# Kernel tuning notes

Hardware: AMD Instinct MI355X
Metric: run time of the kernel (lower is better)

Reference implementation:

```python
import jax, jax.numpy as jnp
import numpy as np

EPS = 1e-8  # torch cosine_similarity clamps norms at 1e-8
TEMPERATURE = 0.05


def _normalize(x):
    n = jnp.linalg.norm(x, axis=-1, keepdims=True)
    return x / jnp.maximum(n, EPS)


def setup_inputs() -> dict:
    key = jax.random.key(0)
    k1, k2, k3 = jax.random.split(key, 3)
    N, D = 8192, 256
    return {
        "text_embeddings": jax.random.normal(k1, (N, D), dtype=jnp.float32),
        "text_pos_embeddings": jax.random.normal(k2, (N, D), dtype=jnp.float32),
        "text_neg_embeddings": jax.random.normal(k3, (N, D), dtype=jnp.float32),
    }


def _pair_loss(a, b):
    # PairInBatchNegCoSentLoss(a, b): cos-sim matrix, scale, diag-subtract, LSE
    sim = _normalize(a) @ _normalize(b).T / TEMPERATURE  # [N, N]
    diff = sim - jnp.diagonal(sim)[:, None]
    return jax.nn.logsumexp(diff, axis=1).mean()


def reference(text_embeddings, text_pos_embeddings, text_neg_embeddings):
    e = _normalize(text_embeddings)
    p = _normalize(text_pos_embeddings)
    n = _normalize(text_neg_embeddings)
    sim_pos = jnp.sum(e * p, axis=-1)          # [N]
    sim_neg = e @ n.T                          # [N, N]
    sim = jnp.concatenate([sim_pos[:, None], sim_neg], axis=1) / TEMPERATURE
    diff = sim - sim[:, 0:1]
    loss = jax.nn.logsumexp(diff, axis=1).mean()
    # add_swap_loss=True: pair loss with (pos, anchor) swapped
    loss = loss + _pair_loss(text_pos_embeddings, text_embeddings)
    return loss
```

## Files before the change

### kernel.cpp

```cpp
#include <hip/hip_runtime.h>
#include <stdint.h>

#define N 8192
#define D 256
#define INV_T 20.0f
#define LOG2E 1.44269504088896340736f
#define BM 128
#define BN 128
#define NXB 64

typedef __attribute__((ext_vector_type(16))) float f32x16;
typedef __attribute__((ext_vector_type(4))) int i32x4;
typedef __attribute__((ext_vector_type(8))) int i32x8;

typedef __attribute__((address_space(3))) uint32_t lds_u32;
typedef __attribute__((address_space(1))) const uint32_t gbl_u32;

static __device__ __forceinline__ float fast_exp2(float x) {
  float r;
  asm("v_exp_f32 %0, %1" : "=v"(r) : "v"(x));
  return r;
}

#define DPP_ADD(v, ctrl)                                                      \
  ((v) + __builtin_bit_cast(float, __builtin_amdgcn_update_dpp(               \
             0, __builtin_bit_cast(int, (v)), (ctrl), 0xf, 0xf, true)))

__global__ __launch_bounds__(256) void normalize_kernel(
    const float* __restrict__ e, const float* __restrict__ p, const float* __restrict__ n,
    uint32_t* __restrict__ eb, uint32_t* __restrict__ pb, uint32_t* __restrict__ nb,
    float* __restrict__ cbuf, float* __restrict__ srow, float* __restrict__ out) {
  const int tid = threadIdx.x;
  const int wave = tid >> 6, lane = tid & 63;
  const int row = blockIdx.x * 4 + wave;

  if (tid < 8) srow[blockIdx.x * 8 + tid] = 0.0f;
  if (blockIdx.x == 0 && tid == 0) out[0] = 0.0f;

  const float4 ev = ((const float4*)(e + (size_t)row * D))[lane];
  const float4 pv = ((const float4*)(p + (size_t)row * D))[lane];
  const float4 nv = ((const float4*)(n + (size_t)row * D))[lane];

  float sse = ev.x*ev.x + ev.y*ev.y + ev.z*ev.z + ev.w*ev.w;
  float ssp = pv.x*pv.x + pv.y*pv.y + pv.z*pv.z + pv.w*pv.w;
  float ssn = nv.x*nv.x + nv.y*nv.y + nv.z*nv.z + nv.w*nv.w;
  float dep = ev.x*pv.x + ev.y*pv.y + ev.z*pv.z + ev.w*pv.w;
#pragma unroll
  for (int m = 1; m < 64; m <<= 1) {
    sse += __shfl_xor(sse, m);
    ssp += __shfl_xor(ssp, m);
    ssn += __shfl_xor(ssn, m);
    dep += __shfl_xor(dep, m);
  }
  const float se = 1.0f / fmaxf(sqrtf(sse), 1e-8f);
  const float sp = 1.0f / fmaxf(sqrtf(ssp), 1e-8f);
  const float sn = 1.0f / fmaxf(sqrtf(ssn), 1e-8f);

  int ue = __builtin_amdgcn_cvt_pk_fp8_f32(ev.x*se, ev.y*se, 0, false);
  ue     = __builtin_amdgcn_cvt_pk_fp8_f32(ev.z*se, ev.w*se, ue, true);
  int up = __builtin_amdgcn_cvt_pk_fp8_f32(pv.x*sp, pv.y*sp, 0, false);
  up     = __builtin_amdgcn_cvt_pk_fp8_f32(pv.z*sp, pv.w*sp, up, true);
  int un = __builtin_amdgcn_cvt_pk_fp8_f32(nv.x*sn, nv.y*sn, 0, false);
  un     = __builtin_amdgcn_cvt_pk_fp8_f32(nv.z*sn, nv.w*sn, un, true);
  eb[row * 64 + lane] = (uint32_t)ue;
  pb[row * 64 + lane] = (uint32_t)up;
  nb[row * 64 + lane] = (uint32_t)un;

  if (lane == 0) cbuf[row] = dep * se * sp * INV_T;
}

__global__ __launch_bounds__(256, 3) void simexp_kernel(
    const uint8_t* __restrict__ eb, const uint8_t* __restrict__ pb,
    const uint8_t* __restrict__ nb, const float* __restrict__ cbuf,
    float* __restrict__ srow) {
  __shared__ uint8_t Bs[BN * D];
  __shared__ float cs[BM];

  const int z = blockIdx.z;
  const uint8_t* __restrict__ A = z ? pb : eb;
  const uint8_t* __restrict__ B = z ? eb : nb;

  const int tid = threadIdx.x;
  const int wave = tid >> 6, lane = tid & 63;
  const int lane31 = lane & 31, half = lane >> 5;
  const int rowTile = blockIdx.x * BM, colblk = blockIdx.y;
  const int colTile = colblk * BN;

#pragma unroll
  for (int i = 0; i < 8; ++i) {
    const int c = i * 256 + tid, r = c >> 4, sl = c & 15;
    const int gg = sl ^ (r & 15);
    __builtin_amdgcn_global_load_lds(
        (gbl_u32*)(B + (size_t)(colTile + r) * D + gg * 16),
        (lds_u32*)&Bs[c * 16], 16, 0, 0);
  }

  const int arow = rowTile + wave * 32 + lane31;
  const uint8_t* __restrict__ Arow = A + (size_t)arow * D + half * 32;
  i32x8 afr[4];
#pragma unroll
  for (int s = 0; s < 4; ++s) {
    const i32x4 lo = *(const i32x4*)(Arow + s * 64);
    const i32x4 hi = *(const i32x4*)(Arow + s * 64 + 16);
    afr[s] = (i32x8){lo[0], lo[1], lo[2], lo[3], hi[0], hi[1], hi[2], hi[3]};
  }

  if (tid < BM) cs[tid] = cbuf[rowTile + tid] * LOG2E;

  int bbase[4];
#pragma unroll
  for (int ni = 0; ni < 4; ++ni) {
    const int cl = ni * 32 + lane31;
    bbase[ni] = (cl << 8) ^ ((cl & 15) << 4) ^ (half << 5);
  }

  f32x16 acc[4];
#pragma unroll
  for (int ni = 0; ni < 4; ++ni)
#pragma unroll
    for (int r = 0; r < 16; ++r) acc[ni][r] = 0.0f;

  __syncthreads();

#pragma unroll
  for (int s = 0; s < 4; ++s) {
#pragma unroll
    for (int ni = 0; ni < 4; ++ni) {
      const int alo = bbase[ni] ^ (s << 6);
      const i32x4 blo = *(const i32x4*)&Bs[alo];
      const i32x4 bhi = *(const i32x4*)&Bs[alo ^ 16];
      const i32x8 b = (i32x8){blo[0], blo[1], blo[2], blo[3],
                              bhi[0], bhi[1], bhi[2], bhi[3]};
      acc[ni] = __builtin_amdgcn_mfma_scale_f32_32x32x64_f8f6f4(
          afr[s], b, acc[ni],
          0 , 0 ,
          0, 0x7F7F7F7F , 0, 0x7F7F7F7F );
    }
  }

  const float K2 = INV_T * LOG2E;
#pragma unroll
  for (int reg = 0; reg < 16; ++reg) {
    const int rlocal = (reg & 3) + 8 * (reg >> 2) + 4 * half;
    const int rowl = wave * 32 + rlocal;
    const float cv = cs[rowl];
    float v = fast_exp2(acc[0][reg] * K2 - cv) + fast_exp2(acc[1][reg] * K2 - cv) +
              fast_exp2(acc[2][reg] * K2 - cv) + fast_exp2(acc[3][reg] * K2 - cv);
    v = DPP_ADD(v, 0xB1);
    v = DPP_ADD(v, 0x4E);
    v = DPP_ADD(v, 0x141);
    v = DPP_ADD(v, 0x140);
    v += __builtin_bit_cast(float, __builtin_amdgcn_ds_swizzle(
             __builtin_bit_cast(int, v), 0x401F));
    if (lane31 == 0)
      atomicAdd(&srow[(size_t)z * N + rowTile + rowl], v);
  }
}

__global__ __launch_bounds__(64) void finalize_kernel(const float* __restrict__ srow,
                                                      float* __restrict__ out) {
  const int r = blockIdx.x * 64 + threadIdx.x;
  const float s = srow[r];
  float val = (r >= N) ? logf(s) : log1pf(s);
#pragma unroll
  for (int m = 1; m < 64; m <<= 1) val += __shfl_xor(val, m);
  if (threadIdx.x == 0) atomicAdd(out, val * (1.0f / (float)N));
}

extern "C" void kernel_launch(void* const* d_in, const int* in_sizes, int n_in,
                              void* d_out, int out_size, void* d_ws, size_t ws_size,
                              hipStream_t stream) {
  const float* e = (const float*)d_in[0];
  const float* p = (const float*)d_in[1];
  const float* n = (const float*)d_in[2];

  char* w = (char*)d_ws;
  uint8_t* eb = (uint8_t*)w;
  uint8_t* pb = eb + (size_t)N * D;
  uint8_t* nb = pb + (size_t)N * D;
  float* cbuf = (float*)(nb + (size_t)N * D);
  float* srow = cbuf + N;

  normalize_kernel<<<N / 4, 256, 0, stream>>>(e, p, n, (uint32_t*)eb, (uint32_t*)pb,
                                              (uint32_t*)nb, cbuf, srow,
                                              (float*)d_out);
  simexp_kernel<<<dim3(N / BM, N / BN, 2), 256, 0, stream>>>(eb, pb, nb, cbuf, srow);
  finalize_kernel<<<256, 64, 0, stream>>>(srow, (float*)d_out);
}
```

Baseline: 126.9 us.

## Replace row-sum atomics with per-column-block partials and restructure MFMA loop

```diff
diff --git a/kernel.cpp b/kernel.cpp
--- a/kernel.cpp
+++ b/kernel.cpp
@@ -29,12 +29,11 @@
 __global__ __launch_bounds__(256) void normalize_kernel(
     const float* __restrict__ e, const float* __restrict__ p, const float* __restrict__ n,
     uint32_t* __restrict__ eb, uint32_t* __restrict__ pb, uint32_t* __restrict__ nb,
-    float* __restrict__ cbuf, float* __restrict__ srow, float* __restrict__ out) {
+    float* __restrict__ cbuf, float* __restrict__ out) {
   const int tid = threadIdx.x;
   const int wave = tid >> 6, lane = tid & 63;
   const int row = blockIdx.x * 4 + wave;
 
-  if (tid < 8) srow[blockIdx.x * 8 + tid] = 0.0f;
   if (blockIdx.x == 0 && tid == 0) out[0] = 0.0f;
 
   const float4 ev = ((const float4*)(e + (size_t)row * D))[lane];
@@ -72,7 +71,7 @@
 __global__ __launch_bounds__(256, 3) void simexp_kernel(
     const uint8_t* __restrict__ eb, const uint8_t* __restrict__ pb,
     const uint8_t* __restrict__ nb, const float* __restrict__ cbuf,
-    float* __restrict__ srow) {
+    float* __restrict__ part) {
   __shared__ uint8_t Bs[BN * D];
   __shared__ float cs[BM];
 
@@ -114,54 +113,65 @@
     bbase[ni] = (cl << 8) ^ ((cl & 15) << 4) ^ (half << 5);
   }
 
-  f32x16 acc[4];
-#pragma unroll
-  for (int ni = 0; ni < 4; ++ni)
-#pragma unroll
-    for (int r = 0; r < 16; ++r) acc[ni][r] = 0.0f;
-
   __syncthreads();
 
+  float cv[16];
 #pragma unroll
-  for (int s = 0; s < 4; ++s) {
+  for (int reg = 0; reg < 16; ++reg)
+    cv[reg] = cs[wave * 32 + (reg & 3) + 8 * (reg >> 2) + 4 * half];
+
+  const float K2 = INV_T * LOG2E;
+  float sums[16];
 #pragma unroll
-    for (int ni = 0; ni < 4; ++ni) {
+  for (int reg = 0; reg < 16; ++reg) sums[reg] = 0.0f;
+
+#pragma unroll
+  for (int ni = 0; ni < 4; ++ni) {
+    f32x16 acc;
+#pragma unroll
+    for (int r = 0; r < 16; ++r) acc[r] = 0.0f;
+#pragma unroll
+    for (int s = 0; s < 4; ++s) {
       const int alo = bbase[ni] ^ (s << 6);
       const i32x4 blo = *(const i32x4*)&Bs[alo];
       const i32x4 bhi = *(const i32x4*)&Bs[alo ^ 16];
       const i32x8 b = (i32x8){blo[0], blo[1], blo[2], blo[3],
                               bhi[0], bhi[1], bhi[2], bhi[3]};
-      acc[ni] = __builtin_amdgcn_mfma_scale_f32_32x32x64_f8f6f4(
-          afr[s], b, acc[ni],
+      acc = __builtin_amdgcn_mfma_scale_f32_32x32x64_f8f6f4(
+          afr[s], b, acc,
           0 , 0 ,
           0, 0x7F7F7F7F , 0, 0x7F7F7F7F );
     }
+#pragma unroll
+    for (int reg = 0; reg < 16; ++reg)
+      sums[reg] += fast_exp2(acc[reg] * K2 - cv[reg]);
   }
 
-  const float K2 = INV_T * LOG2E;
 #pragma unroll
   for (int reg = 0; reg < 16; ++reg) {
-    const int rlocal = (reg & 3) + 8 * (reg >> 2) + 4 * half;
-    const int rowl = wave * 32 + rlocal;
-    const float cv = cs[rowl];
-    float v = fast_exp2(acc[0][reg] * K2 - cv) + fast_exp2(acc[1][reg] * K2 - cv) +
-              fast_exp2(acc[2][reg] * K2 - cv) + fast_exp2(acc[3][reg] * K2 - cv);
+    float v = sums[reg];
     v = DPP_ADD(v, 0xB1);
     v = DPP_ADD(v, 0x4E);
     v = DPP_ADD(v, 0x141);
     v = DPP_ADD(v, 0x140);
     v += __builtin_bit_cast(float, __builtin_amdgcn_ds_swizzle(
              __builtin_bit_cast(int, v), 0x401F));
-    if (lane31 == 0)
-      atomicAdd(&srow[(size_t)z * N + rowTile + rowl], v);
+    if (lane31 == 0) {
+      const int rowl = wave * 32 + (reg & 3) + 8 * (reg >> 2) + 4 * half;
+      part[((size_t)(z * NXB + colblk)) * N + rowTile + rowl] = v;
+    }
   }
 }
 
-__global__ __launch_bounds__(64) void finalize_kernel(const float* __restrict__ srow,
+__global__ __launch_bounds__(64) void finalize_kernel(const float* __restrict__ part,
                                                       float* __restrict__ out) {
   const int r = blockIdx.x * 64 + threadIdx.x;
-  const float s = srow[r];
-  float val = (r >= N) ? logf(s) : log1pf(s);
+  const int z = r >> 13, row = r & (N - 1);
+  float s = 0.0f;
+#pragma unroll 8
+  for (int x = 0; x < NXB; ++x)
+    s += part[((size_t)(z * NXB + x)) * N + row];
+  float val = z ? logf(s) : log1pf(s);
 #pragma unroll
   for (int m = 1; m < 64; m <<= 1) val += __shfl_xor(val, m);
   if (threadIdx.x == 0) atomicAdd(out, val * (1.0f / (float)N));
@@ -179,11 +189,10 @@
   uint8_t* pb = eb + (size_t)N * D;
   uint8_t* nb = pb + (size_t)N * D;
   float* cbuf = (float*)(nb + (size_t)N * D);
-  float* srow = cbuf + N;
+  float* part = cbuf + N;
 
   normalize_kernel<<<N / 4, 256, 0, stream>>>(e, p, n, (uint32_t*)eb, (uint32_t*)pb,
-                                              (uint32_t*)nb, cbuf, srow,
-                                              (float*)d_out);
-  simexp_kernel<<<dim3(N / BM, N / BN, 2), 256, 0, stream>>>(eb, pb, nb, cbuf, srow);
-  finalize_kernel<<<256, 64, 0, stream>>>(srow, (float*)d_out);
+                                              (uint32_t*)nb, cbuf, (float*)d_out);
+  simexp_kernel<<<dim3(N / BM, N / BN, 2), 256, 0, stream>>>(eb, pb, nb, cbuf, part);
+  finalize_kernel<<<256, 64, 0, stream>>>(part, (float*)d_out);
 }
```

Result: slower. 130.0 us (+2.5%).
